# Performance work log

Hardware: AMD Instinct MI355X
Metric: run time of the kernel (lower is better)

## Reference

```python
import jax, jax.numpy as jnp
import numpy as np

N = 100000   # nodes
E = 1600000  # edges
D = 128      # input_dim
H = 128      # hidden_dim
O = 64       # output_dim


def setup_inputs() -> dict:
    key = jax.random.key(0)
    ks = jax.random.split(key, 10)
    x = jax.random.normal(ks[0], (N, D), dtype=jnp.float32)
    edge_index = jax.random.randint(ks[1], (2, E), 0, N, dtype=jnp.int32)

    def glorot(k, fan_in, fan_out):
        lim = np.sqrt(6.0 / (fan_in + fan_out)).astype(np.float32)
        return jax.random.uniform(k, (fan_in, fan_out), jnp.float32, -lim, lim)

    return {
        "x": x,
        "edge_index": edge_index,
        "W0": glorot(ks[2], D, H), "b0": jnp.zeros((H,), jnp.float32),
        "W1": glorot(ks[3], H, H), "b1": jnp.zeros((H,), jnp.float32),
        "W2": glorot(ks[4], H, H), "b2": jnp.zeros((H,), jnp.float32),
        "W3": glorot(ks[5], H, O), "b3": jnp.zeros((O,), jnp.float32),
    }


def gcn_conv(x, src, dst, W, b):
    """PyG GCNConv: out = D^{-1/2} (A + I) D^{-1/2} (x W) + b."""
    n = x.shape[0]
    h = x @ W                                # [N, out]
    loop = jnp.arange(n, dtype=src.dtype)    # self loops
    s = jnp.concatenate([src, loop])
    d = jnp.concatenate([dst, loop])
    deg = jax.ops.segment_sum(jnp.ones_like(d, dtype=h.dtype), d, num_segments=n)
    dinv = jax.lax.rsqrt(jnp.maximum(deg, 1.0))  # deg >= 1 because of self loops
    norm = dinv[s] * dinv[d]                     # [E+N]
    out = jax.ops.segment_sum(h[s] * norm[:, None], d, num_segments=n)
    return out + b


def reference(x, edge_index, W0, b0, W1, b1, W2, b2, W3, b3):
    src, dst = edge_index[0], edge_index[1]
    # three GCNBlocks: GCNConv + ReLU (dropout disabled)
    h = jax.nn.relu(gcn_conv(x, src, dst, W0, b0))
    h = jax.nn.relu(gcn_conv(h, src, dst, W1, b1))
    h = jax.nn.relu(gcn_conv(h, src, dst, W2, b2))
    # final bare GCNConv -> output_dim (no activation)
    return gcn_conv(h, src, dst, W3, b3)
```

## Files before the change

kernel.cpp:

```cpp
#include <hip/hip_runtime.h>
#include <math.h>

#define NN 100000
#define NE 1600000
#define NB 391
#define CAP 5120

typedef __attribute__((ext_vector_type(8))) short short8;
typedef __attribute__((ext_vector_type(4))) float f32x4;
union frag8 { short s[8]; short8 v; };

__device__ __forceinline__ void split_bf16(float a, short& hi, short& lo) {
    unsigned u = __float_as_uint(a);
    unsigned hb = u & 0xffff0000u;
    hi = (short)(hb >> 16);
    float r = a - __uint_as_float(hb);
    unsigned lu = __float_as_uint(r);
    lo = (short)((lu + 0x7fff + ((lu >> 16) & 1)) >> 16);
}

__global__ __launch_bounds__(256) void part2_k(const int* __restrict__ src, const int* __restrict__ dst,
                                               int* bcur, int2* __restrict__ pairs, int e) {
    __shared__ int lhist[NB];
    __shared__ int lbase[NB];
    int t = threadIdx.x;
    for (int i = t; i < NB; i += 256) lhist[i] = 0;
    __syncthreads();
    int e0 = blockIdx.x * 4096;
    int sreg[16], dreg[16];
#pragma unroll
    for (int j = 0; j < 16; ++j) {
        int i = e0 + j * 256 + t;
        if (i < e) {
            sreg[j] = src[i];
            dreg[j] = dst[i];
            atomicAdd(&lhist[dreg[j] >> 8], 1);
        } else dreg[j] = -1;
    }
    __syncthreads();
    for (int i = t; i < NB; i += 256) {
        int c = lhist[i];
        lbase[i] = c ? (i * CAP + atomicAdd(&bcur[i], c)) : 0;
        lhist[i] = 0;
    }
    __syncthreads();
#pragma unroll
    for (int j = 0; j < 16; ++j) {
        if (dreg[j] >= 0) {
            int b = dreg[j] >> 8;
            int pos = lbase[b] + atomicAdd(&lhist[b], 1);
            pairs[pos] = make_int2(sreg[j], dreg[j]);
        }
    }
}

__global__ __launch_bounds__(256) void csr2_k(const int2* __restrict__ pairs, const int* __restrict__ bcur,
                                              float* __restrict__ dinv, int2* __restrict__ rowdesc,
                                              int* __restrict__ csr_src, int n) {
    __shared__ int2 lp[CAP];
    __shared__ int cnt[256];
    __shared__ int wsum[4];
    __shared__ int lcur[256];
    int b = blockIdx.x, t = threadIdx.x;
    const int tot = bcur[b];
    const int e0 = b * CAP;
    cnt[t] = 0;
    __syncthreads();
    for (int e = t; e < tot; e += 256) {
        int2 p = pairs[e0 + e];
        lp[e] = p;
        atomicAdd(&cnt[p.y & 255], 1);
    }
    __syncthreads();
    int c = cnt[t];
    int cp = (c + 3) & ~3;
    int lane = t & 63, wid = t >> 6;
    int inc = cp;
#pragma unroll
    for (int off = 1; off < 64; off <<= 1) {
        int tt = __shfl_up(inc, off);
        if (lane >= off) inc += tt;
    }
    if (lane == 63) wsum[wid] = inc;
    __syncthreads();
    int woff = 0;
    for (int w = 0; w < wid; ++w) woff += wsum[w];
    int excl = inc - cp + woff + e0;
    int i = (b << 8) + t;
    if (i < n) {
        rowdesc[i] = make_int2(excl, cp);
        dinv[i] = 1.0f / sqrtf((float)(c + 1));
    }
    lcur[t] = excl;
    __syncthreads();
    for (int e = t; e < tot; e += 256) {
        int2 p = lp[e];
        int pos = atomicAdd(&lcur[p.y & 255], 1);
        csr_src[pos] = p.x;
    }
    for (int p = c; p < cp; ++p) csr_src[excl + p] = NN;
}

__global__ __launch_bounds__(256) void convw_k(const float* __restrict__ W0, const float* __restrict__ W1,
                                               const float* __restrict__ W2, const float* __restrict__ W3,
                                               short* __restrict__ wt) {
    int gid = blockIdx.x * 256 + threadIdx.x;
    if (gid >= 57344) return;
    const float* W;
    int elem, Ncols, hi_base;
    if (gid < 49152) {
        int w = gid >> 14;
        elem = gid & 16383;
        Ncols = 128;
        W = (w == 0) ? W0 : (w == 1) ? W1 : W2;
        hi_base = w * 32768;
    } else {
        elem = gid - 49152;
        Ncols = 64;
        W = W3;
        hi_base = 98304;
    }
    int k = elem / Ncols, ncol = elem % Ncols;
    short hi, lo;
    split_bf16(W[elem], hi, lo);
    int dstidx = ncol * 128 + k;
    wt[hi_base + dstidx] = hi;
    wt[hi_base + Ncols * 128 + dstidx] = lo;
}

__global__ __launch_bounds__(256) void mfma_gemm_k(const float* __restrict__ A,
                                                   const short* __restrict__ wt_hi,
                                                   const short* __restrict__ wt_lo,
                                                   const float* __restrict__ dinv,
                                                   float* __restrict__ C, int n) {
    constexpr int NT = 8;
    const int tid = threadIdx.x;
    const int wid = tid >> 6, lane = tid & 63;
    const int arow = blockIdx.x * 64 + wid * 16 + (lane & 15);
    const int khalf = lane >> 4;

    f32x4 acc[NT];
#pragma unroll
    for (int nt = 0; nt < NT; ++nt) acc[nt] = (f32x4){0.f, 0.f, 0.f, 0.f};

#pragma unroll
    for (int kc = 0; kc < 4; ++kc) {
        const int k0 = kc * 32 + khalf * 8;
        float4 a0 = make_float4(0.f, 0.f, 0.f, 0.f), a1 = a0;
        if (arow < n) {
            a0 = *(const float4*)(A + (size_t)arow * 128 + k0);
            a1 = *(const float4*)(A + (size_t)arow * 128 + k0 + 4);
        }
        frag8 ahi, alo;
        float av[8] = {a0.x, a0.y, a0.z, a0.w, a1.x, a1.y, a1.z, a1.w};
#pragma unroll
        for (int j = 0; j < 8; ++j) split_bf16(av[j], ahi.s[j], alo.s[j]);

#pragma unroll
        for (int nt = 0; nt < NT; ++nt) {
            const size_t bidx = (size_t)(nt * 16 + (lane & 15)) * 128 + k0;
            short8 bhi = *(const short8*)(wt_hi + bidx);
            short8 blo = *(const short8*)(wt_lo + bidx);
            acc[nt] = __builtin_amdgcn_mfma_f32_16x16x32_bf16(alo.v, bhi, acc[nt], 0, 0, 0);
            acc[nt] = __builtin_amdgcn_mfma_f32_16x16x32_bf16(ahi.v, blo, acc[nt], 0, 0, 0);
            acc[nt] = __builtin_amdgcn_mfma_f32_16x16x32_bf16(ahi.v, bhi, acc[nt], 0, 0, 0);
        }
    }

    const int rbase = blockIdx.x * 64 + wid * 16 + khalf * 4;
    const int col = lane & 15;
    float dv[4];
#pragma unroll
    for (int r = 0; r < 4; ++r) dv[r] = (rbase + r < n) ? dinv[rbase + r] : 0.f;
#pragma unroll
    for (int nt = 0; nt < NT; ++nt) {
#pragma unroll
        for (int r = 0; r < 4; ++r) {
            int row = rbase + r;
            if (row < n) C[(size_t)row * 128 + nt * 16 + col] = acc[nt][r] * dv[r];
        }
    }
}

template<int HOUT>
__global__ __launch_bounds__(256) void fused_k(const float* __restrict__ tmp,
                                               const int* __restrict__ csr_src,
                                               const int2* __restrict__ rowdesc,
                                               const float* __restrict__ dinv,
                                               const float* __restrict__ bias,
                                               const short* __restrict__ wt_hi,
                                               const short* __restrict__ wt_lo,
                                               float* __restrict__ C) {
    constexpr int NT = HOUT / 32;
    __shared__ short Ah[32][136];
    __shared__ short Al[32][136];
    const int t = threadIdx.x;
    const int row0 = blockIdx.x * 32;

    {
        const int l = t & 31;
        const int sub = t >> 5;
        float4 bb = *(const float4*)(bias + l * 4);
        int eptr[4], eend[4];
#pragma unroll
        for (int it = 0; it < 4; ++it) {
            int2 rd = rowdesc[row0 + it * 8 + sub];
            eptr[it] = rd.x;
            eend[it] = rd.x + rd.y;
        }
        int pf = (eptr[0] + l < eend[0]) ? csr_src[eptr[0] + l] : NN;
#pragma unroll
        for (int it = 0; it < 4; ++it) {
            const int node = row0 + it * 8 + sub;
            const float dn = dinv[node];
            float4 acc = *(const float4*)(tmp + (size_t)node * 128 + l * 4);
            int myidx = pf;
            if (it < 3)
                pf = (eptr[it + 1] + l < eend[it + 1]) ? csr_src[eptr[it + 1] + l] : NN;
            int e = eptr[it];
            const int end = eend[it];
            while (e < end) {
                int m = end - e;
                if (m > 32) m = 32;
#pragma unroll 4
                for (int j = 0; j < m; j += 4) {
                    int s0 = __shfl(myidx, j, 32);
                    int s1 = __shfl(myidx, j + 1, 32);
                    int s2 = __shfl(myidx, j + 2, 32);
                    int s3 = __shfl(myidx, j + 3, 32);
                    float4 v0 = *(const float4*)(tmp + (size_t)s0 * 128 + l * 4);
                    float4 v1 = *(const float4*)(tmp + (size_t)s1 * 128 + l * 4);
                    float4 v2 = *(const float4*)(tmp + (size_t)s2 * 128 + l * 4);
                    float4 v3 = *(const float4*)(tmp + (size_t)s3 * 128 + l * 4);
                    acc.x += (v0.x + v1.x) + (v2.x + v3.x);
                    acc.y += (v0.y + v1.y) + (v2.y + v3.y);
                    acc.z += (v0.z + v1.z) + (v2.z + v3.z);
                    acc.w += (v0.w + v1.w) + (v2.w + v3.w);
                }
                e += m;
                if (e < end)
                    myidx = (e + l < end) ? csr_src[e + l] : NN;
            }
            acc.x = fmaxf(fmaf(acc.x, dn, bb.x), 0.f);
            acc.y = fmaxf(fmaf(acc.y, dn, bb.y), 0.f);
            acc.z = fmaxf(fmaf(acc.z, dn, bb.z), 0.f);
            acc.w = fmaxf(fmaf(acc.w, dn, bb.w), 0.f);
            short4 h4, l4;
            split_bf16(acc.x, h4.x, l4.x);
            split_bf16(acc.y, h4.y, l4.y);
            split_bf16(acc.z, h4.z, l4.z);
            split_bf16(acc.w, h4.w, l4.w);
            const int r = it * 8 + sub;
            *(short4*)&Ah[r][l * 4] = h4;
            *(short4*)&Al[r][l * 4] = l4;
        }
    }
    __syncthreads();

    const int wid = t >> 6, lane = t & 63;
    const int rt = wid & 1;
    const int cg = wid >> 1;
    const int arow_l = rt * 16 + (lane & 15);
    const int khalf = lane >> 4;

    f32x4 acc[NT];
#pragma unroll
    for (int nt = 0; nt < NT; ++nt) acc[nt] = (f32x4){0.f, 0.f, 0.f, 0.f};

#pragma unroll
    for (int kc = 0; kc < 4; ++kc) {
        const int k0 = kc * 32 + khalf * 8;
        short8 ahi = *(const short8*)&Ah[arow_l][k0];
        short8 alo = *(const short8*)&Al[arow_l][k0];

#pragma unroll
        for (int nt = 0; nt < NT; ++nt) {
            const size_t bidx = (size_t)(cg * NT * 16 + nt * 16 + (lane & 15)) * 128 + k0;
            short8 bhi = *(const short8*)(wt_hi + bidx);
            short8 blo = *(const short8*)(wt_lo + bidx);
            acc[nt] = __builtin_amdgcn_mfma_f32_16x16x32_bf16(alo, bhi, acc[nt], 0, 0, 0);
            acc[nt] = __builtin_amdgcn_mfma_f32_16x16x32_bf16(ahi, blo, acc[nt], 0, 0, 0);
            acc[nt] = __builtin_amdgcn_mfma_f32_16x16x32_bf16(ahi, bhi, acc[nt], 0, 0, 0);
        }
    }

    const int rbase = row0 + rt * 16 + khalf * 4;
    const int col = lane & 15;
    float dv[4];
#pragma unroll
    for (int r = 0; r < 4; ++r) dv[r] = dinv[rbase + r];
#pragma unroll
    for (int nt = 0; nt < NT; ++nt) {
#pragma unroll
        for (int r = 0; r < 4; ++r) {
            C[(size_t)(rbase + r) * HOUT + cg * NT * 16 + nt * 16 + col] = acc[nt][r] * dv[r];
        }
    }
}

__global__ __launch_bounds__(256) void agg3_k(const float* __restrict__ tmp,
                                              const int* __restrict__ csr_src,
                                              const int2* __restrict__ rowdesc,
                                              const float* __restrict__ dinv,
                                              const float* __restrict__ bias,
                                              float* __restrict__ out) {
    const int t = threadIdx.x;
    const int l = t & 15;
    const int g = t >> 4;
    const int n0 = blockIdx.x * 32 + g * 2;

    float4 bb = *(const float4*)(bias + l * 4);
    int2 rd0 = rowdesc[n0];
    int2 rd1 = rowdesc[n0 + 1];
    int eptr[2] = {rd0.x, rd1.x};
    int eend[2] = {rd0.x + rd0.y, rd1.x + rd1.y};
    int pf = (eptr[0] + l < eend[0]) ? csr_src[eptr[0] + l] : NN;

#pragma unroll
    for (int it = 0; it < 2; ++it) {
        const int node = n0 + it;
        const float dn = dinv[node];
        float4 acc = *(const float4*)(tmp + (size_t)node * 64 + l * 4);
        int myidx = pf;
        if (it < 1)
            pf = (eptr[1] + l < eend[1]) ? csr_src[eptr[1] + l] : NN;
        int e = eptr[it];
        const int end = eend[it];
        while (e < end) {
            int m = end - e;
            if (m > 16) m = 16;
#pragma unroll 4
            for (int j = 0; j < m; j += 4) {
                int s0 = __shfl(myidx, j, 16);
                int s1 = __shfl(myidx, j + 1, 16);
                int s2 = __shfl(myidx, j + 2, 16);
                int s3 = __shfl(myidx, j + 3, 16);
                float4 v0 = *(const float4*)(tmp + (size_t)s0 * 64 + l * 4);
                float4 v1 = *(const float4*)(tmp + (size_t)s1 * 64 + l * 4);
                float4 v2 = *(const float4*)(tmp + (size_t)s2 * 64 + l * 4);
                float4 v3 = *(const float4*)(tmp + (size_t)s3 * 64 + l * 4);
                acc.x += (v0.x + v1.x) + (v2.x + v3.x);
                acc.y += (v0.y + v1.y) + (v2.y + v3.y);
                acc.z += (v0.z + v1.z) + (v2.z + v3.z);
                acc.w += (v0.w + v1.w) + (v2.w + v3.w);
            }
            e += m;
            if (e < end)
                myidx = (e + l < end) ? csr_src[e + l] : NN;
        }
        float4 o;
        o.x = fmaf(acc.x, dn, bb.x);
        o.y = fmaf(acc.y, dn, bb.y);
        o.z = fmaf(acc.z, dn, bb.z);
        o.w = fmaf(acc.w, dn, bb.w);
        *(float4*)(out + (size_t)node * 64 + l * 4) = o;
    }
}

extern "C" void kernel_launch(void* const* d_in, const int* in_sizes, int n_in,
                              void* d_out, int out_size, void* d_ws, size_t ws_size,
                              hipStream_t stream) {
    const float* x    = (const float*)d_in[0];
    const int*   ei   = (const int*)d_in[1];
    const int*   srcp = ei;
    const int*   dstp = ei + NE;
    const float* W0 = (const float*)d_in[2]; const float* b0 = (const float*)d_in[3];
    const float* W1 = (const float*)d_in[4]; const float* b1 = (const float*)d_in[5];
    const float* W2 = (const float*)d_in[6]; const float* b2 = (const float*)d_in[7];
    const float* W3 = (const float*)d_in[8]; const float* b3 = (const float*)d_in[9];
    float* out = (float*)d_out;

    char* ws = (char*)d_ws;
    size_t off = 0;
    auto alloc = [&](size_t bytes) { void* p = ws + off; off = (off + bytes + 255) & ~(size_t)255; return p; };
    int*   bcur    = (int*)alloc((size_t)NB * 4);
    float* dinv    = (float*)alloc((size_t)NN * 4);
    int2*  rowdesc = (int2*)alloc((size_t)NN * 8);
    int*   csr_src = (int*)alloc((size_t)NB * CAP * 4);
    short* wt      = (short*)alloc((size_t)114688 * 2);
    float* bufA    = (float*)alloc((size_t)(NN + 1) * 128 * 4);
    float* bufB    = (float*)alloc((size_t)(NN + 1) * 128 * 4);
    int2*  pairs   = (int2*)bufA;

    const int nblk_e4k = (NE + 4095) / 4096;
    const int nblk_g   = (NN + 63) / 64;
    const int nblk_f   = NN / 32;

    hipMemsetAsync(bufA + (size_t)NN * 128, 0, 512, stream);
    hipMemsetAsync(bufB + (size_t)NN * 128, 0, 512, stream);

    hipMemsetAsync(bcur, 0, (size_t)NB * 4, stream);
    part2_k<<<nblk_e4k, 256, 0, stream>>>(srcp, dstp, bcur, pairs, NE);
    csr2_k<<<NB, 256, 0, stream>>>(pairs, bcur, dinv, rowdesc, csr_src, NN);
    convw_k<<<(57344 + 255) / 256, 256, 0, stream>>>(W0, W1, W2, W3, wt);

    const short* w0h = wt,          *w0l = wt + 16384;
    const short* w1h = wt + 32768,  *w1l = wt + 49152;
    const short* w2h = wt + 65536,  *w2l = wt + 81920;
    const short* w3h = wt + 98304,  *w3l = wt + 106496;

    mfma_gemm_k<<<nblk_g, 256, 0, stream>>>(x, w0h, w0l, dinv, bufB, NN);
    fused_k<128><<<nblk_f, 256, 0, stream>>>(bufB, csr_src, rowdesc, dinv, b0, w1h, w1l, bufA);
    fused_k<128><<<nblk_f, 256, 0, stream>>>(bufA, csr_src, rowdesc, dinv, b1, w2h, w2l, bufB);
    fused_k<64><<<nblk_f, 256, 0, stream>>>(bufB, csr_src, rowdesc, dinv, b2, w3h, w3l, bufA);
    hipMemsetAsync(bufA + (size_t)NN * 64, 0, 256, stream);
    agg3_k<<<nblk_f, 256, 0, stream>>>(bufA, csr_src, rowdesc, dinv, b3, out);
}
```

Baseline: 574.3 us.

## Pack edge pairs into one int and stage first GEMM through shared memory

Edge (src,dst) pairs in the bucketing pass are packed into a single 32-bit int (src<<8 | dst low byte), which halves the pair buffer traffic and the LDS footprint in the CSR build. The first-layer GEMM is rewritten to match the fused kernel's layout: 32-row tiles are loaded coalesced, split into bf16 hi/lo once into shared memory, and four waves split rows and column halves. The old version had each lane split its A fragments directly from strided global loads. This relies on src fitting in 24 bits and on NN being divisible by 32, since bounds checks were removed.

```diff
diff --git a/kernel.cpp b/kernel.cpp
--- a/kernel.cpp
+++ b/kernel.cpp
@@ -8,7 +8,6 @@
 
 typedef __attribute__((ext_vector_type(8))) short short8;
 typedef __attribute__((ext_vector_type(4))) float f32x4;
-union frag8 { short s[8]; short8 v; };
 
 __device__ __forceinline__ void split_bf16(float a, short& hi, short& lo) {
     unsigned u = __float_as_uint(a);
@@ -20,7 +19,7 @@
 }
 
 __global__ __launch_bounds__(256) void part2_k(const int* __restrict__ src, const int* __restrict__ dst,
-                                               int* bcur, int2* __restrict__ pairs, int e) {
+                                               int* bcur, int* __restrict__ pairs, int e) {
     __shared__ int lhist[NB];
     __shared__ int lbase[NB];
     int t = threadIdx.x;
@@ -49,15 +48,15 @@
         if (dreg[j] >= 0) {
             int b = dreg[j] >> 8;
             int pos = lbase[b] + atomicAdd(&lhist[b], 1);
-            pairs[pos] = make_int2(sreg[j], dreg[j]);
-        }
-    }
-}
-
-__global__ __launch_bounds__(256) void csr2_k(const int2* __restrict__ pairs, const int* __restrict__ bcur,
+            pairs[pos] = (sreg[j] << 8) | (dreg[j] & 255);
+        }
+    }
+}
+
+__global__ __launch_bounds__(256) void csr2_k(const int* __restrict__ pairs, const int* __restrict__ bcur,
                                               float* __restrict__ dinv, int2* __restrict__ rowdesc,
                                               int* __restrict__ csr_src, int n) {
-    __shared__ int2 lp[CAP];
+    __shared__ int lp[CAP];
     __shared__ int cnt[256];
     __shared__ int wsum[4];
     __shared__ int lcur[256];
@@ -67,9 +66,9 @@
     cnt[t] = 0;
     __syncthreads();
     for (int e = t; e < tot; e += 256) {
-        int2 p = pairs[e0 + e];
+        int p = pairs[e0 + e];
         lp[e] = p;
-        atomicAdd(&cnt[p.y & 255], 1);
+        atomicAdd(&cnt[p & 255], 1);
     }
     __syncthreads();
     int c = cnt[t];
@@ -94,9 +93,9 @@
     lcur[t] = excl;
     __syncthreads();
     for (int e = t; e < tot; e += 256) {
-        int2 p = lp[e];
-        int pos = atomicAdd(&lcur[p.y & 255], 1);
-        csr_src[pos] = p.x;
+        int p = lp[e];
+        int pos = atomicAdd(&lcur[p & 255], 1);
+        csr_src[pos] = ((unsigned)p) >> 8;
     }
     for (int p = c; p < cp; ++p) csr_src[excl + p] = NN;
 }
@@ -128,56 +127,67 @@
     wt[hi_base + Ncols * 128 + dstidx] = lo;
 }
 
-__global__ __launch_bounds__(256) void mfma_gemm_k(const float* __restrict__ A,
-                                                   const short* __restrict__ wt_hi,
-                                                   const short* __restrict__ wt_lo,
-                                                   const float* __restrict__ dinv,
-                                                   float* __restrict__ C, int n) {
-    constexpr int NT = 8;
-    const int tid = threadIdx.x;
-    const int wid = tid >> 6, lane = tid & 63;
-    const int arow = blockIdx.x * 64 + wid * 16 + (lane & 15);
+__global__ __launch_bounds__(256) void gemm0_k(const float* __restrict__ A,
+                                               const short* __restrict__ wt_hi,
+                                               const short* __restrict__ wt_lo,
+                                               const float* __restrict__ dinv,
+                                               float* __restrict__ C) {
+    __shared__ short Ah[32][136];
+    __shared__ short Al[32][136];
+    const int t = threadIdx.x;
+    const int row0 = blockIdx.x * 32;
+
+#pragma unroll
+    for (int it = 0; it < 4; ++it) {
+        int idx = it * 256 + t;
+        int r = idx >> 5, c4 = idx & 31;
+        float4 v = *(const float4*)(A + (size_t)(row0 + r) * 128 + c4 * 4);
+        short4 h4, l4;
+        split_bf16(v.x, h4.x, l4.x);
+        split_bf16(v.y, h4.y, l4.y);
+        split_bf16(v.z, h4.z, l4.z);
+        split_bf16(v.w, h4.w, l4.w);
+        *(short4*)&Ah[r][c4 * 4] = h4;
+        *(short4*)&Al[r][c4 * 4] = l4;
+    }
+    __syncthreads();
+
+    const int wid = t >> 6, lane = t & 63;
+    const int rt = wid & 1;
+    const int cg = wid >> 1;
+    const int arow_l = rt * 16 + (lane & 15);
     const int khalf = lane >> 4;
 
-    f32x4 acc[NT];
-#pragma unroll
-    for (int nt = 0; nt < NT; ++nt) acc[nt] = (f32x4){0.f, 0.f, 0.f, 0.f};
+    f32x4 acc[4];
+#pragma unroll
+    for (int nt = 0; nt < 4; ++nt) acc[nt] = (f32x4){0.f, 0.f, 0.f, 0.f};
 
 #pragma unroll
     for (int kc = 0; kc < 4; ++kc) {
         const int k0 = kc * 32 + khalf * 8;
-        float4 a0 = make_float4(0.f, 0.f, 0.f, 0.f), a1 = a0;
-        if (arow < n) {
-            a0 = *(const float4*)(A + (size_t)arow * 128 + k0);
-            a1 = *(const float4*)(A + (size_t)arow * 128 + k0 + 4);
-        }
-        frag8 ahi, alo;
-        float av[8] = {a0.x, a0.y, a0.z, a0.w, a1.x, a1.y, a1.z, a1.w};
-#pragma unroll
-        for (int j = 0; j < 8; ++j) split_bf16(av[j], ahi.s[j], alo.s[j]);
-
-#pragma unroll
-        for (int nt = 0; nt < NT; ++nt) {
-            const size_t bidx = (size_t)(nt * 16 + (lane & 15)) * 128 + k0;
+        short8 ahi = *(const short8*)&Ah[arow_l][k0];
+        short8 alo = *(const short8*)&Al[arow_l][k0];
+#pragma unroll
+        for (int nt = 0; nt < 4; ++nt) {
+            const size_t bidx = (size_t)(cg * 64 + nt * 16 + (lane & 15)) * 128 + k0;
             short8 bhi = *(const short8*)(wt_hi + bidx);
             short8 blo = *(const short8*)(wt_lo + bidx);
-            acc[nt] = __builtin_amdgcn_mfma_f32_16x16x32_bf16(alo.v, bhi, acc[nt], 0, 0, 0);
-            acc[nt] = __builtin_amdgcn_mfma_f32_16x16x32_bf16(ahi.v, blo, acc[nt], 0, 0, 0);
-            acc[nt] = __builtin_amdgcn_mfma_f32_16x16x32_bf16(ahi.v, bhi, acc[nt], 0, 0, 0);
-        }
-    }
-
-    const int rbase = blockIdx.x * 64 + wid * 16 + khalf * 4;
+            acc[nt] = __builtin_amdgcn_mfma_f32_16x16x32_bf16(alo, bhi, acc[nt], 0, 0, 0);
+            acc[nt] = __builtin_amdgcn_mfma_f32_16x16x32_bf16(ahi, blo, acc[nt], 0, 0, 0);
+            acc[nt] = __builtin_amdgcn_mfma_f32_16x16x32_bf16(ahi, bhi, acc[nt], 0, 0, 0);
+        }
+    }
+
+    const int rbase = row0 + rt * 16 + khalf * 4;
     const int col = lane & 15;
     float dv[4];
 #pragma unroll
-    for (int r = 0; r < 4; ++r) dv[r] = (rbase + r < n) ? dinv[rbase + r] : 0.f;
-#pragma unroll
-    for (int nt = 0; nt < NT; ++nt) {
+    for (int r = 0; r < 4; ++r) dv[r] = dinv[rbase + r];
+#pragma unroll
+    for (int nt = 0; nt < 4; ++nt) {
 #pragma unroll
         for (int r = 0; r < 4; ++r) {
-            int row = rbase + r;
-            if (row < n) C[(size_t)row * 128 + nt * 16 + col] = acc[nt][r] * dv[r];
+            C[(size_t)(rbase + r) * 128 + cg * 64 + nt * 16 + col] = acc[nt][r] * dv[r];
         }
     }
 }
@@ -272,7 +282,6 @@
         const int k0 = kc * 32 + khalf * 8;
         short8 ahi = *(const short8*)&Ah[arow_l][k0];
         short8 alo = *(const short8*)&Al[arow_l][k0];
-
 #pragma unroll
         for (int nt = 0; nt < NT; ++nt) {
             const size_t bidx = (size_t)(cg * NT * 16 + nt * 16 + (lane & 15)) * 128 + k0;
@@ -380,10 +389,9 @@
     short* wt      = (short*)alloc((size_t)114688 * 2);
     float* bufA    = (float*)alloc((size_t)(NN + 1) * 128 * 4);
     float* bufB    = (float*)alloc((size_t)(NN + 1) * 128 * 4);
-    int2*  pairs   = (int2*)bufA;
+    int*   pairs   = (int*)bufA;
 
     const int nblk_e4k = (NE + 4095) / 4096;
-    const int nblk_g   = (NN + 63) / 64;
     const int nblk_f   = NN / 32;
 
     hipMemsetAsync(bufA + (size_t)NN * 128, 0, 512, stream);
@@ -399,7 +407,7 @@
     const short* w2h = wt + 65536,  *w2l = wt + 81920;
     const short* w3h = wt + 98304,  *w3l = wt + 106496;
 
-    mfma_gemm_k<<<nblk_g, 256, 0, stream>>>(x, w0h, w0l, dinv, bufB, NN);
+    gemm0_k<<<nblk_f, 256, 0, stream>>>(x, w0h, w0l, dinv, bufB);
     fused_k<128><<<nblk_f, 256, 0, stream>>>(bufB, csr_src, rowdesc, dinv, b0, w1h, w1l, bufA);
     fused_k<128><<<nblk_f, 256, 0, stream>>>(bufA, csr_src, rowdesc, dinv, b1, w2h, w2l, bufB);
     fused_k<64><<<nblk_f, 256, 0, stream>>>(bufB, csr_src, rowdesc, dinv, b2, w3h, w3l, bufA);
```

After: 560.4 us. 2.4% less time.
